# Optimization experiments

Measured on AMD Instinct MI355X. Metric: run time of the kernel, lower is better.

The kernel has to match this reference:

```python
import jax, jax.numpy as jnp
import numpy as np

B, S = 4096, 2048
IMU_FREQ = 200
DT = 1.0 / IMU_FREQ


def setup_inputs() -> dict:
    key = jax.random.key(0)
    input_seq = jax.random.normal(key, (B, S, 6), dtype=jnp.float32)
    return {"input_seq": input_seq}


def _skew(v):
    # v: [..., 3] -> [..., 3, 3] skew-symmetric matrix
    x, y, z = v[..., 0], v[..., 1], v[..., 2]
    o = jnp.zeros_like(x)
    return jnp.stack([jnp.stack([o, -z, y], -1),
                      jnp.stack([z, o, -x], -1),
                      jnp.stack([-y, x, o], -1)], -2)


def _axis_angle_into_rotation_matrix(w, dt):
    # w: [B, 3] angular rate; Rodrigues formula with angle = ||w||*dt
    norm = jnp.linalg.norm(w, axis=-1, keepdims=True)            # [B,1]
    angle = (norm * dt)[..., None]                               # [B,1,1]
    axis = w / jnp.maximum(norm, 1e-12)
    K = _skew(axis)                                              # [B,3,3]
    I = jnp.eye(3, dtype=w.dtype)
    return I + jnp.sin(angle) * K + (1.0 - jnp.cos(angle)) * (K @ K)


def reference(input_seq):
    dt = jnp.asarray(DT, dtype=input_seq.dtype)
    half_dt2 = dt * dt * 0.5  # (delta_t/2)*delta_t
    w = jnp.swapaxes(input_seq[..., :3], 0, 1)              # [S,B,3]
    a = jnp.swapaxes(input_seq[..., 3:], 0, 1)[..., None]   # [S,B,3,1]
    Bn = input_seq.shape[0]

    def step(carry, inp):
        dr, dv, dp = carry
        wk, ak = inp
        dr = dr @ _axis_angle_into_rotation_matrix(wk, dt)
        dv = dv + dr @ (ak * dt)
        dp = dp + dv * dt + dr @ (ak * half_dt2)
        return (dr, dv, dp), None

    I0 = jnp.broadcast_to(jnp.eye(3, dtype=input_seq.dtype), (Bn, 3, 3))
    z0 = jnp.zeros((Bn, 3, 1), dtype=input_seq.dtype)
    (dr, dv, dp), _ = jax.lax.scan(step, (I0, z0, z0), (w, a))

    # rotation matrix -> axis-angle -> quaternion [qw, qx, qy, qz]
    tr = dr[..., 0, 0] + dr[..., 1, 1] + dr[..., 2, 2]
    angle = jnp.arccos(jnp.clip((tr - 1.0) * 0.5, -1.0 + 1e-7, 1.0 - 1e-7))
    denom = jnp.maximum(2.0 * jnp.sin(angle), 1e-12)[..., None]
    axis = jnp.stack([dr[..., 2, 1] - dr[..., 1, 2],
                      dr[..., 0, 2] - dr[..., 2, 0],
                      dr[..., 1, 0] - dr[..., 0, 1]], -1) / denom
    half = angle * 0.5
    quat = jnp.concatenate([jnp.cos(half)[..., None],
                            axis * jnp.sin(half)[..., None]], axis=-1)  # [B,4]
    return jnp.concatenate([dp[..., 0], quat], axis=-1)  # [B,7]
```

## Files before the change

### kernel.cpp

```cpp
#include <hip/hip_runtime.h>
#include <math.h>

#define S_LEN 2048
#define B_TOT 4096
#define CHUNK 16
constexpr float DT       = 1.0f / 200.0f;
constexpr float HALF_DT2 = DT * DT * 0.5f;

__device__ __forceinline__ void istep(
    float& R00, float& R01, float& R02,
    float& R10, float& R11, float& R12,
    float& R20, float& R21, float& R22,
    float& Vx, float& Vy, float& Vz,
    float& Px, float& Py, float& Pz,
    float wx, float wy, float wz, float ax, float ay, float az)
{
    const float ux = wx * DT, uy = wy * DT, uz = wz * DT;
    const float t2 = ux * ux + uy * uy + uz * uz;
    const float Ac = 1.0f + t2 * (-1.0f / 6.0f  + t2 * (1.0f / 120.0f));
    const float Bc = 0.5f + t2 * (-1.0f / 24.0f + t2 * (1.0f / 720.0f));

    const float K00 = 1.0f + Bc * (ux * ux - t2);
    const float K11 = 1.0f + Bc * (uy * uy - t2);
    const float K22 = 1.0f + Bc * (uz * uz - t2);
    const float bxy = Bc * ux * uy, bxz = Bc * ux * uz, byz = Bc * uy * uz;
    const float aux = Ac * ux, auy = Ac * uy, auz = Ac * uz;
    const float K01 = bxy - auz, K10 = bxy + auz;
    const float K02 = bxz + auy, K20 = bxz - auy;
    const float K12 = byz - aux, K21 = byz + aux;

    float r0, r1, r2;
    r0 = R00 * K00 + R01 * K10 + R02 * K20;
    r1 = R00 * K01 + R01 * K11 + R02 * K21;
    r2 = R00 * K02 + R01 * K12 + R02 * K22;
    R00 = r0; R01 = r1; R02 = r2;
    r0 = R10 * K00 + R11 * K10 + R12 * K20;
    r1 = R10 * K01 + R11 * K11 + R12 * K21;
    r2 = R10 * K02 + R11 * K12 + R12 * K22;
    R10 = r0; R11 = r1; R12 = r2;
    r0 = R20 * K00 + R21 * K10 + R22 * K20;
    r1 = R20 * K01 + R21 * K11 + R22 * K21;
    r2 = R20 * K02 + R21 * K12 + R22 * K22;
    R20 = r0; R21 = r1; R22 = r2;

    const float tx = R00 * ax + R01 * ay + R02 * az;
    const float ty = R10 * ax + R11 * ay + R12 * az;
    const float tz = R20 * ax + R21 * ay + R22 * az;
    Vx += tx * DT; Vy += ty * DT; Vz += tz * DT;
    Px += Vx * DT + tx * HALF_DT2;
    Py += Vy * DT + ty * HALF_DT2;
    Pz += Vz * DT + tz * HALF_DT2;
}

__global__ __launch_bounds__(256, 4)
void preint_kernel(const float* __restrict__ in, float* __restrict__ out)
{
    const int slot = threadIdx.x >> 7;
    const int b    = blockIdx.x * 2 + slot;
    const int tid  = threadIdx.x & 127;
    const int lane = threadIdx.x & 63;
    const int half = (threadIdx.x >> 6) & 1;

    __shared__ float stx[2][15];

    const float4* gp = reinterpret_cast<const float4*>(in)
                     + (size_t)b * (S_LEN * 6 / 4) + (size_t)tid * 24;

    float4 a0 = gp[0], a1 = gp[1], a2 = gp[2];
    float4 b0 = gp[3], b1 = gp[4], b2 = gp[5];

    float R00 = 1.f, R01 = 0.f, R02 = 0.f;
    float R10 = 0.f, R11 = 1.f, R12 = 0.f;
    float R20 = 0.f, R21 = 0.f, R22 = 1.f;
    float Vx = 0.f, Vy = 0.f, Vz = 0.f;
    float Px = 0.f, Py = 0.f, Pz = 0.f;

    #pragma unroll 1
    for (int p = 0; p < 8; p += 2) {
        istep(R00,R01,R02,R10,R11,R12,R20,R21,R22,Vx,Vy,Vz,Px,Py,Pz,
              a0.x, a0.y, a0.z, a0.w, a1.x, a1.y);
        istep(R00,R01,R02,R10,R11,R12,R20,R21,R22,Vx,Vy,Vz,Px,Py,Pz,
              a1.z, a1.w, a2.x, a2.y, a2.z, a2.w);
        if (p < 6) { a0 = gp[6]; a1 = gp[7]; a2 = gp[8]; }

        istep(R00,R01,R02,R10,R11,R12,R20,R21,R22,Vx,Vy,Vz,Px,Py,Pz,
              b0.x, b0.y, b0.z, b0.w, b1.x, b1.y);
        istep(R00,R01,R02,R10,R11,R12,R20,R21,R22,Vx,Vy,Vz,Px,Py,Pz,
              b1.z, b1.w, b2.x, b2.y, b2.z, b2.w);
        if (p < 6) { b0 = gp[9]; b1 = gp[10]; b2 = gp[11]; gp += 6; }
    }

    #pragma unroll
    for (int o = 1; o < 64; o <<= 1) {
        const float Tb = (float)(o * CHUNK) * DT;
        const float S00 = __shfl_down(R00, o, 64), S01 = __shfl_down(R01, o, 64), S02 = __shfl_down(R02, o, 64);
        const float S10 = __shfl_down(R10, o, 64), S11 = __shfl_down(R11, o, 64), S12 = __shfl_down(R12, o, 64);
        const float S20 = __shfl_down(R20, o, 64), S21 = __shfl_down(R21, o, 64), S22 = __shfl_down(R22, o, 64);
        const float Wx  = __shfl_down(Vx, o, 64),  Wy  = __shfl_down(Vy, o, 64),  Wz  = __shfl_down(Vz, o, 64);
        const float Qx  = __shfl_down(Px, o, 64),  Qy  = __shfl_down(Py, o, 64),  Qz  = __shfl_down(Pz, o, 64);

        const float nPx = Px + Vx * Tb + R00 * Qx + R01 * Qy + R02 * Qz;
        const float nPy = Py + Vy * Tb + R10 * Qx + R11 * Qy + R12 * Qz;
        const float nPz = Pz + Vz * Tb + R20 * Qx + R21 * Qy + R22 * Qz;
        const float nVx = Vx + R00 * Wx + R01 * Wy + R02 * Wz;
        const float nVy = Vy + R10 * Wx + R11 * Wy + R12 * Wz;
        const float nVz = Vz + R20 * Wx + R21 * Wy + R22 * Wz;
        float r0, r1, r2;
        r0 = R00 * S00 + R01 * S10 + R02 * S20;
        r1 = R00 * S01 + R01 * S11 + R02 * S21;
        r2 = R00 * S02 + R01 * S12 + R02 * S22;
        R00 = r0; R01 = r1; R02 = r2;
        r0 = R10 * S00 + R11 * S10 + R12 * S20;
        r1 = R10 * S01 + R11 * S11 + R12 * S21;
        r2 = R10 * S02 + R11 * S12 + R12 * S22;
        R10 = r0; R11 = r1; R12 = r2;
        r0 = R20 * S00 + R21 * S10 + R22 * S20;
        r1 = R20 * S01 + R21 * S11 + R22 * S21;
        r2 = R20 * S02 + R21 * S12 + R22 * S22;
        R20 = r0; R21 = r1; R22 = r2;

        Px = nPx; Py = nPy; Pz = nPz;
        Vx = nVx; Vy = nVy; Vz = nVz;
    }

    if (lane == 0 && half == 1) {
        float* s = stx[slot];
        s[0]=R00; s[1]=R01; s[2]=R02; s[3]=R10; s[4]=R11; s[5]=R12;
        s[6]=R20; s[7]=R21; s[8]=R22; s[9]=Vx; s[10]=Vy; s[11]=Vz;
        s[12]=Px; s[13]=Py; s[14]=Pz;
    }
    __syncthreads();

    if (tid == 0) {
        const float* s = stx[slot];
        const float S00=s[0],S01=s[1],S02=s[2],S10=s[3],S11=s[4],S12=s[5];
        const float S20=s[6],S21=s[7],S22=s[8],Wx=s[9],Wy=s[10],Wz=s[11];
        const float Qx=s[12],Qy=s[13],Qz=s[14];
        const float Tb = (float)(64 * CHUNK) * DT;

        const float nPx = Px + Vx * Tb + R00 * Qx + R01 * Qy + R02 * Qz;
        const float nPy = Py + Vy * Tb + R10 * Qx + R11 * Qy + R12 * Qz;
        const float nPz = Pz + Vz * Tb + R20 * Qx + R21 * Qy + R22 * Qz;
        float r0, r1, r2;
        r0 = R00 * S00 + R01 * S10 + R02 * S20;
        r1 = R00 * S01 + R01 * S11 + R02 * S21;
        r2 = R00 * S02 + R01 * S12 + R02 * S22;
        const float F00 = r0, F01 = r1, F02 = r2;
        r0 = R10 * S00 + R11 * S10 + R12 * S20;
        r1 = R10 * S01 + R11 * S11 + R12 * S21;
        r2 = R10 * S02 + R11 * S12 + R12 * S22;
        const float F10 = r0, F11 = r1, F12 = r2;
        r0 = R20 * S00 + R21 * S10 + R22 * S20;
        r1 = R20 * S01 + R21 * S11 + R22 * S21;
        r2 = R20 * S02 + R21 * S12 + R22 * S22;
        const float F20 = r0, F21 = r1, F22 = r2;

        const float tr = F00 + F11 + F22;
        float c = (tr - 1.0f) * 0.5f;
        c = fminf(fmaxf(c, -1.0f + 1e-7f), 1.0f - 1e-7f);
        const float angle = acosf(c);
        const float sden = fmaxf(2.0f * sinf(angle), 1e-12f);
        const float axx = (F21 - F12) / sden;
        const float ayy = (F02 - F20) / sden;
        const float azz = (F10 - F01) / sden;
        const float halfang = angle * 0.5f;
        const float sh = sinf(halfang), ch = cosf(halfang);
        float* o = out + (size_t)b * 7;
        o[0] = nPx; o[1] = nPy; o[2] = nPz;
        o[3] = ch;
        o[4] = axx * sh; o[5] = ayy * sh; o[6] = azz * sh;
    }
}

extern "C" void kernel_launch(void* const* d_in, const int* in_sizes, int n_in,
                              void* d_out, int out_size, void* d_ws, size_t ws_size,
                              hipStream_t stream)
{
    const float* in = (const float*)d_in[0];
    float* out = (float*)d_out;
    const int threads = 256;
    const int blocks = B_TOT / 2;
    preint_kernel<<<blocks, threads, 0, stream>>>(in, out);
}
```

Before: 51.03 us.

## Stage coalesced global loads through LDS transpose instead of strided per-thread loads

Each thread used to read its own contiguous 16-step chunk straight from global memory, which leaves wide strides between lanes. Now each wave loads the batch row in lane-contiguous order, issuing twelve float4 loads per half. It transposes the data through a padded LDS buffer (13-float4 row stride to limit bank conflicts) so each thread can read its chunk back. The second half is prefetched into registers while the first half is computed. This raises register and LDS use, and the launch-bounds occupancy hint is lowered from 4 to 2 to match.

```diff
diff --git a/kernel.cpp b/kernel.cpp
--- a/kernel.cpp
+++ b/kernel.cpp
@@ -52,7 +52,7 @@
     Pz += Vz * DT + tz * HALF_DT2;
 }
 
-__global__ __launch_bounds__(256, 4)
+__global__ __launch_bounds__(256, 2)
 void preint_kernel(const float* __restrict__ in, float* __restrict__ out)
 {
     const int slot = threadIdx.x >> 7;
@@ -60,14 +60,36 @@
     const int tid  = threadIdx.x & 127;
     const int lane = threadIdx.x & 63;
     const int half = (threadIdx.x >> 6) & 1;
-
+    const int wv   = threadIdx.x >> 6;
+
+    __shared__ float4 lds[4][64 * 13];
     __shared__ float stx[2][15];
 
-    const float4* gp = reinterpret_cast<const float4*>(in)
-                     + (size_t)b * (S_LEN * 6 / 4) + (size_t)tid * 24;
-
-    float4 a0 = gp[0], a1 = gp[1], a2 = gp[2];
-    float4 b0 = gp[3], b1 = gp[4], b2 = gp[5];
+    const float4* g4 = reinterpret_cast<const float4*>(in) + (size_t)b * (S_LEN * 6 / 4);
+
+    int goff[12], loff[12];
+    #pragma unroll
+    for (int m = 0; m < 12; ++m) {
+        const int s   = m * 64 + lane;
+        const int rec = s / 12;
+        const int j   = s - 12 * rec;
+        goff[m] = (half * 64 + rec) * 24 + j;
+        loff[m] = rec * 13 + j;
+    }
+    float4* L = &lds[wv][0];
+    const int rbase = lane * 13;
+
+    float4 v[12];
+    #pragma unroll
+    for (int m = 0; m < 12; ++m) v[m] = g4[goff[m]];
+    #pragma unroll
+    for (int m = 0; m < 12; ++m) L[loff[m]] = v[m];
+
+    #pragma unroll
+    for (int m = 0; m < 12; ++m) v[m] = g4[goff[m] + 12];
+
+    asm volatile("s_waitcnt lgkmcnt(0)" ::: "memory");
+    __builtin_amdgcn_sched_barrier(0);
 
     float R00 = 1.f, R01 = 0.f, R02 = 0.f;
     float R10 = 0.f, R11 = 1.f, R12 = 0.f;
@@ -75,19 +97,35 @@
     float Vx = 0.f, Vy = 0.f, Vz = 0.f;
     float Px = 0.f, Py = 0.f, Pz = 0.f;
 
-    #pragma unroll 1
-    for (int p = 0; p < 8; p += 2) {
-        istep(R00,R01,R02,R10,R11,R12,R20,R21,R22,Vx,Vy,Vz,Px,Py,Pz,
-              a0.x, a0.y, a0.z, a0.w, a1.x, a1.y);
-        istep(R00,R01,R02,R10,R11,R12,R20,R21,R22,Vx,Vy,Vz,Px,Py,Pz,
-              a1.z, a1.w, a2.x, a2.y, a2.z, a2.w);
-        if (p < 6) { a0 = gp[6]; a1 = gp[7]; a2 = gp[8]; }
-
-        istep(R00,R01,R02,R10,R11,R12,R20,R21,R22,Vx,Vy,Vz,Px,Py,Pz,
-              b0.x, b0.y, b0.z, b0.w, b1.x, b1.y);
-        istep(R00,R01,R02,R10,R11,R12,R20,R21,R22,Vx,Vy,Vz,Px,Py,Pz,
-              b1.z, b1.w, b2.x, b2.y, b2.z, b2.w);
-        if (p < 6) { b0 = gp[9]; b1 = gp[10]; b2 = gp[11]; gp += 6; }
+    #pragma unroll
+    for (int t = 0; t < 4; ++t) {
+        const float4 q0 = L[rbase + 3 * t];
+        const float4 q1 = L[rbase + 3 * t + 1];
+        const float4 q2 = L[rbase + 3 * t + 2];
+        istep(R00,R01,R02,R10,R11,R12,R20,R21,R22,Vx,Vy,Vz,Px,Py,Pz,
+              q0.x, q0.y, q0.z, q0.w, q1.x, q1.y);
+        istep(R00,R01,R02,R10,R11,R12,R20,R21,R22,Vx,Vy,Vz,Px,Py,Pz,
+              q1.z, q1.w, q2.x, q2.y, q2.z, q2.w);
+    }
+
+    asm volatile("s_waitcnt lgkmcnt(0)" ::: "memory");
+    __builtin_amdgcn_sched_barrier(0);
+
+    #pragma unroll
+    for (int m = 0; m < 12; ++m) L[loff[m]] = v[m];
+
+    asm volatile("s_waitcnt lgkmcnt(0)" ::: "memory");
+    __builtin_amdgcn_sched_barrier(0);
+
+    #pragma unroll
+    for (int t = 0; t < 4; ++t) {
+        const float4 q0 = L[rbase + 3 * t];
+        const float4 q1 = L[rbase + 3 * t + 1];
+        const float4 q2 = L[rbase + 3 * t + 2];
+        istep(R00,R01,R02,R10,R11,R12,R20,R21,R22,Vx,Vy,Vz,Px,Py,Pz,
+              q0.x, q0.y, q0.z, q0.w, q1.x, q1.y);
+        istep(R00,R01,R02,R10,R11,R12,R20,R21,R22,Vx,Vy,Vz,Px,Py,Pz,
+              q1.z, q1.w, q2.x, q2.y, q2.z, q2.w);
     }
 
     #pragma unroll
```

New measurement: 46.43 us, median of 2. 1.1x faster.
